# Optimization experiments

Hardware: AMD Instinct MI355X
Metric: run time of the kernel (lower is better)

Reference implementation:

```python
import jax, jax.numpy as jnp
import numpy as np

# Faithful reference for NaiveKmeans._cost / one assignment step of forward:
# squared Euclidean distances (torch.cdist(x, centers)**2) followed by a
# row-wise min (costs) and argmin (cluster indices).
# Note: the original module's host-side while-loop re-seeds centers as
# x[indices] (shape (N,d)), which is a bug that explodes to an NxN cdist;
# the kernel-relevant, well-defined math is this single cdist^2 + min step,
# which we implement here (it is exactly what forward computes before the loop).

def setup_inputs() -> dict:
    key = jax.random.key(0)
    kx, kc = jax.random.split(key)
    x = jax.random.normal(kx, (131072, 128), dtype=jnp.float32)
    centers = jax.random.normal(kc, (1024, 128), dtype=jnp.float32)
    return {"x": x, "centers": centers}


def _sq_cdist(x, c):
    x2 = jnp.sum(x * x, axis=1, keepdims=True)        # [N, 1]
    c2 = jnp.sum(c * c, axis=1)                       # [K]
    d2 = x2 + c2 - 2.0 * (x @ c.T)                    # [N, K]
    return jnp.maximum(d2, 0.0)


def reference(x, centers):
    d2 = _sq_cdist(x, centers)          # [N, K] squared distances
    costs = jnp.min(d2, axis=1)         # [N] per-point cost
    indices = jnp.argmin(d2, axis=1)    # [N] cluster assignment
    return costs, indices
```

## Files before the change

kernel.cpp:

```cpp
#include <hip/hip_runtime.h>


typedef _Float16 f16x8 __attribute__((ext_vector_type(8)));
typedef float    f32x4 __attribute__((ext_vector_type(4)));
typedef unsigned short u16;

constexpr int N = 131072, D = 128, K = 1024;
constexpr int MT = 128;

union H2U { _Float16 h; unsigned short u; };

__device__ inline void gl_lds16(const void* g, void* l) {
  __builtin_amdgcn_global_load_lds(
      (const __attribute__((address_space(1))) unsigned int*)g,
      (__attribute__((address_space(3))) unsigned int*)l, 16, 0, 0);
}

__global__ void prep_centers(const float* __restrict__ centers,
                             u16* __restrict__ Bh, u16* __restrict__ Bl,
                             float* __restrict__ c2) {
  const int wave = threadIdx.x >> 6, lane = threadIdx.x & 63;
  const int c = blockIdx.x * 4 + wave;
  const float2 v = ((const float2*)(centers + (size_t)c * D))[lane];
  float s = v.x * v.x + v.y * v.y;
  #pragma unroll
  for (int off = 32; off; off >>= 1) s += __shfl_xor(s, off, 64);
  if (lane == 0) c2[c] = s;

  H2U h0, h1, l0, l1;
  h0.h = (_Float16)v.x;  l0.h = (_Float16)(v.x - (float)h0.h);
  h1.h = (_Float16)v.y;  l1.h = (_Float16)(v.y - (float)h1.h);
  const int cb = c >> 7, cm = c & 127;
  const int kc = lane >> 4, q = (lane >> 2) & 3, j0 = (lane & 3) * 2;
  const size_t off = (((size_t)(cb * 4 + kc) * 4 + q) * 128 + cm) * 8 + j0;
  *(unsigned*)(Bh + off) = (unsigned)h0.u | ((unsigned)h1.u << 16);
  *(unsigned*)(Bl + off) = (unsigned)l0.u | ((unsigned)l1.u << 16);
}

__global__ __launch_bounds__(256, 2) void kmeans_mfma(
    const float* __restrict__ x,
    const u16* __restrict__ Bh_g, const u16* __restrict__ Bl_g,
    const float* __restrict__ c2g,
    float* __restrict__ out_cost, float* __restrict__ out_idx)
{
  __shared__ __align__(16) u16 smem[40960];
  u16* Ah = smem;
  u16* Al = smem + 16384;

  const int tid = threadIdx.x;
  const int wave = tid >> 6, lane = tid & 63;
  const int wr = wave >> 1, wc = wave & 1;
  const int q = lane >> 4, ln = lane & 15;
  const int m0 = blockIdx.x * MT;

  #pragma unroll
  for (int i = 0; i < 16; ++i) {
    const int flat = i * 256 + tid;
    const int m = flat >> 5, c4 = flat & 31, k0 = c4 * 4;
    const float4 v = *(const float4*)(x + (size_t)(m0 + m) * D + k0);
    const int kc = k0 >> 5, qq = (k0 >> 3) & 3, j0 = k0 & 7;
    const float vv[4] = {v.x, v.y, v.z, v.w};
    H2U h[4], l[4];
    #pragma unroll
    for (int z = 0; z < 4; ++z) {
      h[z].h = (_Float16)vv[z];
      l[z].h = (_Float16)(vv[z] - (float)h[z].h);
    }
    const int off = ((kc * 4 + qq) * 128 + m) * 8 + j0;
    uint2 hp, lp;
    hp.x = h[0].u | ((unsigned)h[1].u << 16); hp.y = h[2].u | ((unsigned)h[3].u << 16);
    lp.x = l[0].u | ((unsigned)l[1].u << 16); lp.y = l[2].u | ((unsigned)l[3].u << 16);
    *(uint2*)(Ah + off) = hp;
    *(uint2*)(Al + off) = lp;
  }
  __syncthreads();

  float x2m = 0.f;
  if (tid < MT) {
    #pragma unroll
    for (int kq = 0; kq < 16; ++kq) {
      const f16x8 hv = *(const f16x8*)(Ah + (kq * 128 + tid) * 8);
      const f16x8 lv = *(const f16x8*)(Al + (kq * 128 + tid) * 8);
      #pragma unroll
      for (int e = 0; e < 8; ++e) {
        const float xv = (float)hv[e] + (float)lv[e];
        x2m += xv * xv;
      }
    }
  }

  auto stageBh = [&](int cc, int p) {
    const size_t gbase = (size_t)cc * 4096;
    u16* buf = smem + 32768 + p * 4096;
    #pragma unroll
    for (int i = 0; i < 2; ++i) {
      const size_t eoff = (size_t)i * 2048 + (size_t)wave * 512;
      gl_lds16(Bh_g + gbase + eoff + (size_t)lane * 8, buf + eoff);
    }
  };
  auto blPtr = [&](int cc, int t) {
    return (const f16x8*)(Bl_g +
        ((size_t)(cc * 4 + q) * 128 + wc * 64 + t * 16 + ln) * 8);
  };

  float bestV[16]; int bestI[16];
  #pragma unroll
  for (int b = 0; b < 16; ++b) { bestV[b] = 3.4e38f; bestI[b] = 0; }

  stageBh(0, 0);
  f16x8 blc[4], bln[4];
  #pragma unroll
  for (int t = 0; t < 4; ++t) blc[t] = *blPtr(0, t);

  for (int ct = 0; ct < 8; ++ct) {
    f32x4 acc[4][4];
    #pragma unroll
    for (int mt = 0; mt < 4; ++mt)
      #pragma unroll
      for (int nt = 0; nt < 4; ++nt)
        acc[mt][nt] = (f32x4){0.f, 0.f, 0.f, 0.f};

    float c2v[4];
    #pragma unroll
    for (int nt = 0; nt < 4; ++nt)
      c2v[nt] = c2g[ct * 128 + wc * 64 + nt * 16 + ln];

    #pragma unroll
    for (int kc = 0; kc < 4; ++kc) {
      const int cc = ct * 4 + kc;
      __syncthreads();
      if (cc < 31) {
        stageBh(cc + 1, (cc + 1) & 1);
        #pragma unroll
        for (int t = 0; t < 4; ++t) bln[t] = *blPtr(cc + 1, t);
      }
      const u16* buf = smem + 32768 + (cc & 1) * 4096;

      f16x8 ah[4], al[4], bh[4];
      #pragma unroll
      for (int t = 0; t < 4; ++t) {
        const int moff = ((kc * 4 + q) * 128 + wr * 64 + t * 16 + ln) * 8;
        ah[t] = *(const f16x8*)(Ah + moff);
        al[t] = *(const f16x8*)(Al + moff);
        bh[t] = *(const f16x8*)(buf + (q * 128 + wc * 64 + t * 16 + ln) * 8);
      }
      #pragma unroll
      for (int mt = 0; mt < 4; ++mt)
        #pragma unroll
        for (int nt = 0; nt < 4; ++nt)
          acc[mt][nt] = __builtin_amdgcn_mfma_f32_16x16x32_f16(ah[mt], bh[nt], acc[mt][nt], 0, 0, 0);
      #pragma unroll
      for (int mt = 0; mt < 4; ++mt)
        #pragma unroll
        for (int nt = 0; nt < 4; ++nt)
          acc[mt][nt] = __builtin_amdgcn_mfma_f32_16x16x32_f16(al[mt], bh[nt], acc[mt][nt], 0, 0, 0);
      #pragma unroll
      for (int mt = 0; mt < 4; ++mt)
        #pragma unroll
        for (int nt = 0; nt < 4; ++nt)
          acc[mt][nt] = __builtin_amdgcn_mfma_f32_16x16x32_f16(ah[mt], blc[nt], acc[mt][nt], 0, 0, 0);
      #pragma unroll
      for (int t = 0; t < 4; ++t) blc[t] = bln[t];
    }

    #pragma unroll
    for (int nt = 0; nt < 4; ++nt) {
      const int n = ct * 128 + wc * 64 + nt * 16 + ln;
      #pragma unroll
      for (int mt = 0; mt < 4; ++mt)
        #pragma unroll
        for (int r = 0; r < 4; ++r) {
          const float s = __builtin_fmaf(-2.f, acc[mt][nt][r], c2v[nt]);
          const int b = mt * 4 + r;
          if (s < bestV[b]) { bestV[b] = s; bestI[b] = n; }
        }
    }
  }

  #pragma unroll
  for (int b = 0; b < 16; ++b) {
    float v = bestV[b]; int idx = bestI[b];
    #pragma unroll
    for (int off = 1; off < 16; off <<= 1) {
      const float ov = __shfl_xor(v, off, 64);
      const int   oi = __shfl_xor(idx, off, 64);
      if (ov < v || (ov == v && oi < idx)) { v = ov; idx = oi; }
    }
    bestV[b] = v; bestI[b] = idx;
  }

  __syncthreads();
  float* redV = (float*)(smem + 32768);
  int*   redI = (int*)(smem + 33280);
  if (ln == 0) {
    #pragma unroll
    for (int b = 0; b < 16; ++b) {
      const int ml = wr * 64 + (b >> 2) * 16 + q * 4 + (b & 3);
      redV[ml * 2 + wc] = bestV[b];
      redI[ml * 2 + wc] = bestI[b];
    }
  }
  __syncthreads();
  if (tid < MT) {
    float v = redV[tid * 2]; int idx = redI[tid * 2];
    const float v1 = redV[tid * 2 + 1]; const int i1 = redI[tid * 2 + 1];
    if (v1 < v || (v1 == v && i1 < idx)) { v = v1; idx = i1; }
    float cost = x2m + v;
    if (cost < 0.f) cost = 0.f;
    out_cost[m0 + tid] = cost;
    out_idx[m0 + tid]  = (float)idx;
  }
}

extern "C" void kernel_launch(void* const* d_in, const int* in_sizes, int n_in,
                              void* d_out, int out_size, void* d_ws, size_t ws_size,
                              hipStream_t stream) {
  const float* x       = (const float*)d_in[0];
  const float* centers = (const float*)d_in[1];
  u16*   Bh = (u16*)d_ws;
  u16*   Bl = Bh + (size_t)K * D;
  float* c2 = (float*)(Bl + (size_t)K * D);
  float* out_cost = (float*)d_out;
  float* out_idx  = out_cost + N;

  prep_centers<<<K / 4, 256, 0, stream>>>(centers, Bh, Bl, c2);
  kmeans_mfma<<<N / MT, 256, 0, stream>>>(x, Bh, Bl, c2, out_cost, out_idx);
}
```

Baseline: 179.4 us.

## Software-pipeline MFMA groups with register double-buffered B and A fragment reads

```diff
diff --git a/kernel.cpp b/kernel.cpp
--- a/kernel.cpp
+++ b/kernel.cpp
@@ -98,84 +98,115 @@
       gl_lds16(Bh_g + gbase + eoff + (size_t)lane * 8, buf + eoff);
     }
   };
-  auto blPtr = [&](int cc, int t) {
-    return (const f16x8*)(Bl_g +
-        ((size_t)(cc * 4 + q) * 128 + wc * 64 + t * 16 + ln) * 8);
-  };
 
   float bestV[16]; int bestI[16];
   #pragma unroll
   for (int b = 0; b < 16; ++b) { bestV[b] = 3.4e38f; bestI[b] = 0; }
 
+  f32x4 acc[4][4];
+  #pragma unroll
+  for (int mt = 0; mt < 4; ++mt)
+    #pragma unroll
+    for (int nt = 0; nt < 4; ++nt)
+      acc[mt][nt] = (f32x4){0.f, 0.f, 0.f, 0.f};
+
+  f16x8 ah[4], al[4];
+  f16x8 bhS[2][4], blS[2][4];
+
+#define READ_B(J, CC)  do {                                                    \
+    const u16* buf_ = smem + 32768 + ((J) & 1) * 4096;                         \
+    _Pragma("unroll")                                                          \
+    for (int t = 0; t < 4; ++t) {                                              \
+      bhS[(J) & 1][t] =                                                        \
+          *(const f16x8*)(buf_ + (q * 128 + wc * 64 + t * 16 + ln) * 8);       \
+      blS[(J) & 1][t] = *(const f16x8*)(Bl_g +                                 \
+          ((size_t)((CC) * 4 + q) * 128 + wc * 64 + t * 16 + ln) * 8);         \
+    }                                                                          \
+  } while (0)
+
+#define READ_A(KC)  do {                                                       \
+    _Pragma("unroll")                                                          \
+    for (int t = 0; t < 4; ++t) {                                              \
+      const int aoff_ = (((KC) * 4 + q) * 128 + wr * 64 + t * 16 + ln) * 8;    \
+      ah[t] = *(const f16x8*)(Ah + aoff_);                                     \
+      al[t] = *(const f16x8*)(Al + aoff_);                                     \
+    }                                                                          \
+  } while (0)
+
+#define MFMA_GROUP(MS)  do {                                                   \
+    _Pragma("unroll")                                                          \
+    for (int mt = 0; mt < 4; ++mt)                                             \
+      _Pragma("unroll")                                                        \
+      for (int nt = 0; nt < 4; ++nt)                                           \
+        acc[mt][nt] = __builtin_amdgcn_mfma_f32_16x16x32_f16(                  \
+            ah[mt], bhS[MS][nt], acc[mt][nt], 0, 0, 0);                        \
+    _Pragma("unroll")                                                          \
+    for (int mt = 0; mt < 4; ++mt)                                             \
+      _Pragma("unroll")                                                        \
+      for (int nt = 0; nt < 4; ++nt)                                           \
+        acc[mt][nt] = __builtin_amdgcn_mfma_f32_16x16x32_f16(                  \
+            al[mt], bhS[MS][nt], acc[mt][nt], 0, 0, 0);                        \
+    _Pragma("unroll")                                                          \
+    for (int mt = 0; mt < 4; ++mt)                                             \
+      _Pragma("unroll")                                                        \
+      for (int nt = 0; nt < 4; ++nt)                                           \
+        acc[mt][nt] = __builtin_amdgcn_mfma_f32_16x16x32_f16(                  \
+            ah[mt], blS[MS][nt], acc[mt][nt], 0, 0, 0);                        \
+  } while (0)
+
+#define EPILOGUE(G)  do {                                                      \
+    _Pragma("unroll")                                                          \
+    for (int nt = 0; nt < 4; ++nt) {                                           \
+      const int n_ = (G) * 128 + wc * 64 + nt * 16 + ln;                       \
+      const float c2v_ = c2g[n_];                                              \
+      _Pragma("unroll")                                                        \
+      for (int mt = 0; mt < 4; ++mt)                                           \
+        _Pragma("unroll")                                                      \
+        for (int r = 0; r < 4; ++r) {                                          \
+          const float s_ = __builtin_fmaf(-2.f, acc[mt][nt][r], c2v_);         \
+          const int b_ = mt * 4 + r;                                           \
+          if (s_ < bestV[b_]) { bestV[b_] = s_; bestI[b_] = n_; }              \
+        }                                                                      \
+    }                                                                          \
+    _Pragma("unroll")                                                          \
+    for (int mt = 0; mt < 4; ++mt)                                             \
+      _Pragma("unroll")                                                        \
+      for (int nt = 0; nt < 4; ++nt)                                           \
+        acc[mt][nt] = (f32x4){0.f, 0.f, 0.f, 0.f};                             \
+  } while (0)
+
   stageBh(0, 0);
-  f16x8 blc[4], bln[4];
-  #pragma unroll
-  for (int t = 0; t < 4; ++t) blc[t] = *blPtr(0, t);
-
-  for (int ct = 0; ct < 8; ++ct) {
-    f32x4 acc[4][4];
-    #pragma unroll
-    for (int mt = 0; mt < 4; ++mt)
-      #pragma unroll
-      for (int nt = 0; nt < 4; ++nt)
-        acc[mt][nt] = (f32x4){0.f, 0.f, 0.f, 0.f};
-
-    float c2v[4];
-    #pragma unroll
-    for (int nt = 0; nt < 4; ++nt)
-      c2v[nt] = c2g[ct * 128 + wc * 64 + nt * 16 + ln];
-
-    #pragma unroll
-    for (int kc = 0; kc < 4; ++kc) {
-      const int cc = ct * 4 + kc;
-      __syncthreads();
-      if (cc < 31) {
-        stageBh(cc + 1, (cc + 1) & 1);
-        #pragma unroll
-        for (int t = 0; t < 4; ++t) bln[t] = *blPtr(cc + 1, t);
-      }
-      const u16* buf = smem + 32768 + (cc & 1) * 4096;
-
-      f16x8 ah[4], al[4], bh[4];
-      #pragma unroll
-      for (int t = 0; t < 4; ++t) {
-        const int moff = ((kc * 4 + q) * 128 + wr * 64 + t * 16 + ln) * 8;
-        ah[t] = *(const f16x8*)(Ah + moff);
-        al[t] = *(const f16x8*)(Al + moff);
-        bh[t] = *(const f16x8*)(buf + (q * 128 + wc * 64 + t * 16 + ln) * 8);
-      }
-      #pragma unroll
-      for (int mt = 0; mt < 4; ++mt)
-        #pragma unroll
-        for (int nt = 0; nt < 4; ++nt)
-          acc[mt][nt] = __builtin_amdgcn_mfma_f32_16x16x32_f16(ah[mt], bh[nt], acc[mt][nt], 0, 0, 0);
-      #pragma unroll
-      for (int mt = 0; mt < 4; ++mt)
-        #pragma unroll
-        for (int nt = 0; nt < 4; ++nt)
-          acc[mt][nt] = __builtin_amdgcn_mfma_f32_16x16x32_f16(al[mt], bh[nt], acc[mt][nt], 0, 0, 0);
-      #pragma unroll
-      for (int mt = 0; mt < 4; ++mt)
-        #pragma unroll
-        for (int nt = 0; nt < 4; ++nt)
-          acc[mt][nt] = __builtin_amdgcn_mfma_f32_16x16x32_f16(ah[mt], blc[nt], acc[mt][nt], 0, 0, 0);
-      #pragma unroll
-      for (int t = 0; t < 4; ++t) blc[t] = bln[t];
-    }
-
-    #pragma unroll
-    for (int nt = 0; nt < 4; ++nt) {
-      const int n = ct * 128 + wc * 64 + nt * 16 + ln;
-      #pragma unroll
-      for (int mt = 0; mt < 4; ++mt)
-        #pragma unroll
-        for (int r = 0; r < 4; ++r) {
-          const float s = __builtin_fmaf(-2.f, acc[mt][nt][r], c2v[nt]);
-          const int b = mt * 4 + r;
-          if (s < bestV[b]) { bestV[b] = s; bestI[b] = n; }
-        }
-    }
-  }
+
+  for (int it = 0; it < 8; ++it) {
+    const int c0 = it * 4;
+    __syncthreads();
+    stageBh(c0 + 1, 1);
+    READ_B(0, c0);
+    if (it > 0) { MFMA_GROUP(1); EPILOGUE(it - 1); }
+    READ_A(0);
+    __syncthreads();
+    stageBh(c0 + 2, 0);
+    READ_B(1, c0 + 1);
+    MFMA_GROUP(0);
+    READ_A(1);
+    __syncthreads();
+    stageBh(c0 + 3, 1);
+    READ_B(0, c0 + 2);
+    MFMA_GROUP(1);
+    READ_A(2);
+    __syncthreads();
+    if (it < 7) stageBh(c0 + 4, 0);
+    READ_B(1, c0 + 3);
+    MFMA_GROUP(0);
+    READ_A(3);
+  }
+  MFMA_GROUP(1);
+  EPILOGUE(7);
+
+#undef READ_B
+#undef READ_A
+#undef MFMA_GROUP
+#undef EPILOGUE
 
   #pragma unroll
   for (int b = 0; b < 16; ++b) {
```

Measured after the change: 180.2 us. Within noise of the previous version (+0.5%).

## Use single-pass fp16 GEMM with error-bound filter and exact rescan of ambiguous rows

Applied to the files above, without the earlier changes.

```diff
diff --git a/kernel.cpp b/kernel.cpp
--- a/kernel.cpp
+++ b/kernel.cpp
@@ -4,6 +4,7 @@
 typedef _Float16 f16x8 __attribute__((ext_vector_type(8)));
 typedef float    f32x4 __attribute__((ext_vector_type(4)));
 typedef unsigned short u16;
+typedef unsigned int   u32;
 
 constexpr int N = 131072, D = 128, K = 1024;
 constexpr int MT = 128;
@@ -18,18 +19,28 @@
 
 __global__ void prep_centers(const float* __restrict__ centers,
                              u16* __restrict__ Bh, u16* __restrict__ Bl,
-                             float* __restrict__ c2) {
+                             float* __restrict__ c2, u32* __restrict__ scal) {
   const int wave = threadIdx.x >> 6, lane = threadIdx.x & 63;
   const int c = blockIdx.x * 4 + wave;
   const float2 v = ((const float2*)(centers + (size_t)c * D))[lane];
-  float s = v.x * v.x + v.y * v.y;
+
+  H2U h0, h1, l0, l1;
+  h0.h = (_Float16)v.x;  float r0 = v.x - (float)h0.h;  l0.h = (_Float16)r0;
+  h1.h = (_Float16)v.y;  float r1 = v.y - (float)h1.h;  l1.h = (_Float16)r1;
+
+  float s  = v.x * v.x + v.y * v.y;
+  float sl = r0 * r0 + r1 * r1;
   #pragma unroll
-  for (int off = 32; off; off >>= 1) s += __shfl_xor(s, off, 64);
-  if (lane == 0) c2[c] = s;
-
-  H2U h0, h1, l0, l1;
-  h0.h = (_Float16)v.x;  l0.h = (_Float16)(v.x - (float)h0.h);
-  h1.h = (_Float16)v.y;  l1.h = (_Float16)(v.y - (float)h1.h);
+  for (int off = 32; off; off >>= 1) {
+    s  += __shfl_xor(s, off, 64);
+    sl += __shfl_xor(sl, off, 64);
+  }
+  if (lane == 0) {
+    c2[c] = s;
+    atomicMax(&scal[0], __float_as_uint(s));
+    atomicMax(&scal[1], __float_as_uint(sl));
+  }
+
   const int cb = c >> 7, cm = c & 127;
   const int kc = lane >> 4, q = (lane >> 2) & 3, j0 = (lane & 3) * 2;
   const size_t off = (((size_t)(cb * 4 + kc) * 4 + q) * 128 + cm) * 8 + j0;
@@ -37,15 +48,15 @@
   *(unsigned*)(Bl + off) = (unsigned)l0.u | ((unsigned)l1.u << 16);
 }
 
-__global__ __launch_bounds__(256, 2) void kmeans_mfma(
-    const float* __restrict__ x,
-    const u16* __restrict__ Bh_g, const u16* __restrict__ Bl_g,
-    const float* __restrict__ c2g,
+__global__ void __launch_bounds__(256, 3) kmeans_p1(
+    const float* __restrict__ x, const u16* __restrict__ Bh_g,
+    const float* __restrict__ c2g, const u32* __restrict__ scal,
+    u32* __restrict__ cnt, u32* __restrict__ worklist,
     float* __restrict__ out_cost, float* __restrict__ out_idx)
 {
-  __shared__ __align__(16) u16 smem[40960];
-  u16* Ah = smem;
-  u16* Al = smem + 16384;
+  __shared__ __align__(16) u16 Ah[16384];
+  __shared__ float x2l[128], Ml[128];
+  __shared__ float redA[256]; __shared__ int redB[256]; __shared__ float redC[256];
 
   const int tid = threadIdx.x;
   const int wave = tid >> 6, lane = tid & 63;
@@ -53,64 +64,53 @@
   const int q = lane >> 4, ln = lane & 15;
   const int m0 = blockIdx.x * MT;
 
+  const float cmax  = sqrtf(__uint_as_float(scal[0]));
+  const float clmax = sqrtf(__uint_as_float(scal[1]));
+
+  {
+    const int m = tid >> 1, half = (tid & 1) * 64;
+    const float* xrow = x + (size_t)(m0 + m) * D + half;
+    float x2p = 0.f, xl2p = 0.f;
+    #pragma unroll
+    for (int i = 0; i < 16; ++i) {
+      const float4 v = *(const float4*)(xrow + i * 4);
+      const int k0 = half + i * 4;
+      const int kq = k0 >> 5, qq = (k0 >> 3) & 3, j0 = k0 & 7;
+      const float vv[4] = {v.x, v.y, v.z, v.w};
+      H2U h[4];
+      #pragma unroll
+      for (int z = 0; z < 4; ++z) {
+        h[z].h = (_Float16)vv[z];
+        const float l = vv[z] - (float)h[z].h;
+        x2p  += vv[z] * vv[z];
+        xl2p += l * l;
+      }
+      uint2 hp;
+      hp.x = h[0].u | ((unsigned)h[1].u << 16);
+      hp.y = h[2].u | ((unsigned)h[3].u << 16);
+      *(uint2*)(Ah + ((kq * 4 + qq) * 128 + m) * 8 + j0) = hp;
+    }
+    const float ox2 = __shfl_xor(x2p, 1, 64);
+    const float oxl = __shfl_xor(xl2p, 1, 64);
+    if ((tid & 1) == 0) {
+      const float X2 = x2p + ox2, XL2 = xl2p + oxl;
+      x2l[m] = X2;
+      const float xn = sqrtf(X2), xln = sqrtf(XL2);
+      Ml[m] = 4.f * (xln * cmax + xn * clmax + xln * clmax) + 0.05f;
+    }
+  }
+  __syncthreads();
+
+  const size_t laneB = ((size_t)q * 128 + wc * 64 + ln) * 8;
+  const u16* bhP = Bh_g + laneB;
+
+  float v1[16], v2[16]; int i1[16];
   #pragma unroll
-  for (int i = 0; i < 16; ++i) {
-    const int flat = i * 256 + tid;
-    const int m = flat >> 5, c4 = flat & 31, k0 = c4 * 4;
-    const float4 v = *(const float4*)(x + (size_t)(m0 + m) * D + k0);
-    const int kc = k0 >> 5, qq = (k0 >> 3) & 3, j0 = k0 & 7;
-    const float vv[4] = {v.x, v.y, v.z, v.w};
-    H2U h[4], l[4];
-    #pragma unroll
-    for (int z = 0; z < 4; ++z) {
-      h[z].h = (_Float16)vv[z];
-      l[z].h = (_Float16)(vv[z] - (float)h[z].h);
-    }
-    const int off = ((kc * 4 + qq) * 128 + m) * 8 + j0;
-    uint2 hp, lp;
-    hp.x = h[0].u | ((unsigned)h[1].u << 16); hp.y = h[2].u | ((unsigned)h[3].u << 16);
-    lp.x = l[0].u | ((unsigned)l[1].u << 16); lp.y = l[2].u | ((unsigned)l[3].u << 16);
-    *(uint2*)(Ah + off) = hp;
-    *(uint2*)(Al + off) = lp;
-  }
-  __syncthreads();
-
-  float x2m = 0.f;
-  if (tid < MT) {
-    #pragma unroll
-    for (int kq = 0; kq < 16; ++kq) {
-      const f16x8 hv = *(const f16x8*)(Ah + (kq * 128 + tid) * 8);
-      const f16x8 lv = *(const f16x8*)(Al + (kq * 128 + tid) * 8);
-      #pragma unroll
-      for (int e = 0; e < 8; ++e) {
-        const float xv = (float)hv[e] + (float)lv[e];
-        x2m += xv * xv;
-      }
-    }
-  }
-
-  auto stageBh = [&](int cc, int p) {
-    const size_t gbase = (size_t)cc * 4096;
-    u16* buf = smem + 32768 + p * 4096;
-    #pragma unroll
-    for (int i = 0; i < 2; ++i) {
-      const size_t eoff = (size_t)i * 2048 + (size_t)wave * 512;
-      gl_lds16(Bh_g + gbase + eoff + (size_t)lane * 8, buf + eoff);
-    }
-  };
-  auto blPtr = [&](int cc, int t) {
-    return (const f16x8*)(Bl_g +
-        ((size_t)(cc * 4 + q) * 128 + wc * 64 + t * 16 + ln) * 8);
-  };
-
-  float bestV[16]; int bestI[16];
+  for (int b = 0; b < 16; ++b) { v1[b] = 3.4e38f; v2[b] = 3.4e38f; i1[b] = 0; }
+
+  f16x8 bhS[2][4];
   #pragma unroll
-  for (int b = 0; b < 16; ++b) { bestV[b] = 3.4e38f; bestI[b] = 0; }
-
-  stageBh(0, 0);
-  f16x8 blc[4], bln[4];
-  #pragma unroll
-  for (int t = 0; t < 4; ++t) blc[t] = *blPtr(0, t);
+  for (int t = 0; t < 4; ++t) bhS[0][t] = *(const f16x8*)(bhP + t * 128);
 
   for (int ct = 0; ct < 8; ++ct) {
     f32x4 acc[4][4];
@@ -128,39 +128,22 @@
     #pragma unroll
     for (int kc = 0; kc < 4; ++kc) {
       const int cc = ct * 4 + kc;
-      __syncthreads();
-      if (cc < 31) {
-        stageBh(cc + 1, (cc + 1) & 1);
-        #pragma unroll
-        for (int t = 0; t < 4; ++t) bln[t] = *blPtr(cc + 1, t);
-      }
-      const u16* buf = smem + 32768 + (cc & 1) * 4096;
-
-      f16x8 ah[4], al[4], bh[4];
-      #pragma unroll
-      for (int t = 0; t < 4; ++t) {
-        const int moff = ((kc * 4 + q) * 128 + wr * 64 + t * 16 + ln) * 8;
-        ah[t] = *(const f16x8*)(Ah + moff);
-        al[t] = *(const f16x8*)(Al + moff);
-        bh[t] = *(const f16x8*)(buf + (q * 128 + wc * 64 + t * 16 + ln) * 8);
-      }
+      const int cur = kc & 1, nxt = cur ^ 1;
+      if (kc < 3 || ct < 7) {
+        const size_t goff = (size_t)(cc + 1) * 4096;
+        #pragma unroll
+        for (int t = 0; t < 4; ++t)
+          bhS[nxt][t] = *(const f16x8*)(bhP + goff + t * 128);
+      }
+      f16x8 ah[4];
+      #pragma unroll
+      for (int t = 0; t < 4; ++t)
+        ah[t] = *(const f16x8*)(Ah + ((kc * 4 + q) * 128 + wr * 64 + t * 16 + ln) * 8);
       #pragma unroll
       for (int mt = 0; mt < 4; ++mt)
         #pragma unroll
         for (int nt = 0; nt < 4; ++nt)
-          acc[mt][nt] = __builtin_amdgcn_mfma_f32_16x16x32_f16(ah[mt], bh[nt], acc[mt][nt], 0, 0, 0);
-      #pragma unroll
-      for (int mt = 0; mt < 4; ++mt)
-        #pragma unroll
-        for (int nt = 0; nt < 4; ++nt)
-          acc[mt][nt] = __builtin_amdgcn_mfma_f32_16x16x32_f16(al[mt], bh[nt], acc[mt][nt], 0, 0, 0);
-      #pragma unroll
-      for (int mt = 0; mt < 4; ++mt)
-        #pragma unroll
-        for (int nt = 0; nt < 4; ++nt)
-          acc[mt][nt] = __builtin_amdgcn_mfma_f32_16x16x32_f16(ah[mt], blc[nt], acc[mt][nt], 0, 0, 0);
-      #pragma unroll
-      for (int t = 0; t < 4; ++t) blc[t] = bln[t];
+          acc[mt][nt] = __builtin_amdgcn_mfma_f32_16x16x32_f16(ah[mt], bhS[cur][nt], acc[mt][nt], 0, 0, 0);
     }
 
     #pragma unroll
@@ -172,43 +155,245 @@
         for (int r = 0; r < 4; ++r) {
           const float s = __builtin_fmaf(-2.f, acc[mt][nt][r], c2v[nt]);
           const int b = mt * 4 + r;
-          if (s < bestV[b]) { bestV[b] = s; bestI[b] = n; }
+          if (s < v1[b]) { v2[b] = v1[b]; v1[b] = s; i1[b] = n; }
+          else if (s < v2[b]) v2[b] = s;
         }
     }
   }
 
   #pragma unroll
   for (int b = 0; b < 16; ++b) {
-    float v = bestV[b]; int idx = bestI[b];
+    float a1 = v1[b], a2 = v2[b]; int ai = i1[b];
     #pragma unroll
     for (int off = 1; off < 16; off <<= 1) {
-      const float ov = __shfl_xor(v, off, 64);
-      const int   oi = __shfl_xor(idx, off, 64);
-      if (ov < v || (ov == v && oi < idx)) { v = ov; idx = oi; }
-    }
-    bestV[b] = v; bestI[b] = idx;
-  }
-
-  __syncthreads();
-  float* redV = (float*)(smem + 32768);
-  int*   redI = (int*)(smem + 33280);
+      const float o1 = __shfl_xor(a1, off, 64);
+      const float o2 = __shfl_xor(a2, off, 64);
+      const int   oi = __shfl_xor(ai, off, 64);
+      float n2;
+      if (o1 < a1 || (o1 == a1 && oi < ai)) { n2 = fminf(a1, o2); a1 = o1; ai = oi; }
+      else                                   { n2 = fminf(o1, a2); }
+      a2 = n2;
+    }
+    v1[b] = a1; v2[b] = a2; i1[b] = ai;
+  }
   if (ln == 0) {
     #pragma unroll
     for (int b = 0; b < 16; ++b) {
       const int ml = wr * 64 + (b >> 2) * 16 + q * 4 + (b & 3);
-      redV[ml * 2 + wc] = bestV[b];
-      redI[ml * 2 + wc] = bestI[b];
+      redA[ml * 2 + wc] = v1[b];
+      redB[ml * 2 + wc] = i1[b];
+      redC[ml * 2 + wc] = v2[b];
     }
   }
   __syncthreads();
   if (tid < MT) {
-    float v = redV[tid * 2]; int idx = redI[tid * 2];
-    const float v1 = redV[tid * 2 + 1]; const int i1 = redI[tid * 2 + 1];
-    if (v1 < v || (v1 == v && i1 < idx)) { v = v1; idx = i1; }
-    float cost = x2m + v;
+    float a1 = redA[tid * 2], a2 = redC[tid * 2]; int ai = redB[tid * 2];
+    const float o1 = redA[tid * 2 + 1], o2 = redC[tid * 2 + 1];
+    const int   oi = redB[tid * 2 + 1];
+    float n2;
+    if (o1 < a1 || (o1 == a1 && oi < ai)) { n2 = fminf(a1, o2); a1 = o1; ai = oi; }
+    else                                   { n2 = fminf(o1, a2); }
+    a2 = n2;
+
+    float cost = x2l[tid] + a1;
     if (cost < 0.f) cost = 0.f;
     out_cost[m0 + tid] = cost;
-    out_idx[m0 + tid]  = (float)idx;
+    out_idx[m0 + tid]  = (float)ai;
+    if (a2 <= a1 + Ml[tid]) {
+      const u32 slot = atomicAdd(cnt, 1u);
+      worklist[slot] = (u32)(m0 + tid);
+    }
+  }
+}
+
+__global__ void __launch_bounds__(256, 2) kmeans_rescan(
+    const float* __restrict__ x,
+    const u16* __restrict__ Bh_g, const u16* __restrict__ Bl_g,
+    const float* __restrict__ c2g, const u32* __restrict__ cnt,
+    const u32* __restrict__ worklist,
+    float* __restrict__ out_cost, float* __restrict__ out_idx)
+{
+  __shared__ __align__(16) u16 smem[40960];
+  __shared__ int pidl[128];
+  u16* Ah = smem;
+  u16* Al = smem + 16384;
+
+  const int tid = threadIdx.x;
+  const int wave = tid >> 6, lane = tid & 63;
+  const int wr = wave >> 1, wc = wave & 1;
+  const int q = lane >> 4, ln = lane & 15;
+  const int count = (int)cnt[0];
+
+  for (int g = blockIdx.x; ; g += 128) {
+    const int base = g * MT;
+    if (base >= count) break;
+    __syncthreads();
+    if (tid < 128) {
+      int wi = base + tid; if (wi >= count) wi = count - 1;
+      pidl[tid] = (int)worklist[wi];
+    }
+    __syncthreads();
+
+    #pragma unroll
+    for (int i = 0; i < 16; ++i) {
+      const int flat = i * 256 + tid;
+      const int m = flat >> 5, c4 = flat & 31, k0 = c4 * 4;
+      const float4 v = *(const float4*)(x + (size_t)pidl[m] * D + k0);
+      const int kc = k0 >> 5, qq = (k0 >> 3) & 3, j0 = k0 & 7;
+      const float vv[4] = {v.x, v.y, v.z, v.w};
+      H2U h[4], l[4];
+      #pragma unroll
+      for (int z = 0; z < 4; ++z) {
+        h[z].h = (_Float16)vv[z];
+        l[z].h = (_Float16)(vv[z] - (float)h[z].h);
+      }
+      const int off = ((kc * 4 + qq) * 128 + m) * 8 + j0;
+      uint2 hp, lp;
+      hp.x = h[0].u | ((unsigned)h[1].u << 16); hp.y = h[2].u | ((unsigned)h[3].u << 16);
+      lp.x = l[0].u | ((unsigned)l[1].u << 16); lp.y = l[2].u | ((unsigned)l[3].u << 16);
+      *(uint2*)(Ah + off) = hp;
+      *(uint2*)(Al + off) = lp;
+    }
+    __syncthreads();
+
+    float x2m = 0.f;
+    if (tid < 128) {
+      #pragma unroll
+      for (int kq = 0; kq < 16; ++kq) {
+        const f16x8 hv = *(const f16x8*)(Ah + (kq * 128 + tid) * 8);
+        const f16x8 lv = *(const f16x8*)(Al + (kq * 128 + tid) * 8);
+        #pragma unroll
+        for (int e = 0; e < 8; ++e) {
+          const float xv = (float)hv[e] + (float)lv[e];
+          x2m += xv * xv;
+        }
+      }
+    }
+
+    const size_t laneB = ((size_t)q * 128 + wc * 64 + ln) * 8;
+    const u16* blP = Bl_g + laneB;
+
+    float bestV[16]; int bestI[16];
+    #pragma unroll
+    for (int b = 0; b < 16; ++b) { bestV[b] = 3.4e38f; bestI[b] = 0; }
+
+    {
+      const size_t eoffb = (size_t)wave * 512;
+      #pragma unroll
+      for (int i = 0; i < 2; ++i)
+        gl_lds16(Bh_g + (size_t)i * 2048 + eoffb + (size_t)lane * 8,
+                 smem + 32768 + i * 2048 + eoffb);
+    }
+    f16x8 blc[4], bln[4];
+    #pragma unroll
+    for (int t = 0; t < 4; ++t) blc[t] = *(const f16x8*)(blP + t * 128);
+
+    for (int ct = 0; ct < 8; ++ct) {
+      f32x4 acc[4][4];
+      #pragma unroll
+      for (int mt = 0; mt < 4; ++mt)
+        #pragma unroll
+        for (int nt = 0; nt < 4; ++nt)
+          acc[mt][nt] = (f32x4){0.f, 0.f, 0.f, 0.f};
+
+      float c2v[4];
+      #pragma unroll
+      for (int nt = 0; nt < 4; ++nt)
+        c2v[nt] = c2g[ct * 128 + wc * 64 + nt * 16 + ln];
+
+      #pragma unroll
+      for (int kc = 0; kc < 4; ++kc) {
+        const int cc = ct * 4 + kc;
+        __syncthreads();
+        if (cc < 31) {
+          const size_t gbase = (size_t)(cc + 1) * 4096;
+          u16* buf = smem + 32768 + ((cc + 1) & 1) * 4096;
+          const size_t eoffb = (size_t)wave * 512;
+          #pragma unroll
+          for (int i = 0; i < 2; ++i)
+            gl_lds16(Bh_g + gbase + (size_t)i * 2048 + eoffb + (size_t)lane * 8,
+                     buf + i * 2048 + eoffb);
+          #pragma unroll
+          for (int t = 0; t < 4; ++t)
+            bln[t] = *(const f16x8*)(blP + gbase + t * 128);
+        }
+        const u16* buf = smem + 32768 + (cc & 1) * 4096;
+
+        f16x8 ah[4], al[4], bh[4];
+        #pragma unroll
+        for (int t = 0; t < 4; ++t) {
+          const int moff = ((kc * 4 + q) * 128 + wr * 64 + t * 16 + ln) * 8;
+          ah[t] = *(const f16x8*)(Ah + moff);
+          al[t] = *(const f16x8*)(Al + moff);
+          bh[t] = *(const f16x8*)(buf + (q * 128 + wc * 64 + t * 16 + ln) * 8);
+        }
+        #pragma unroll
+        for (int mt = 0; mt < 4; ++mt)
+          #pragma unroll
+          for (int nt = 0; nt < 4; ++nt)
+            acc[mt][nt] = __builtin_amdgcn_mfma_f32_16x16x32_f16(ah[mt], bh[nt], acc[mt][nt], 0, 0, 0);
+        #pragma unroll
+        for (int mt = 0; mt < 4; ++mt)
+          #pragma unroll
+          for (int nt = 0; nt < 4; ++nt)
+            acc[mt][nt] = __builtin_amdgcn_mfma_f32_16x16x32_f16(al[mt], bh[nt], acc[mt][nt], 0, 0, 0);
+        #pragma unroll
+        for (int mt = 0; mt < 4; ++mt)
+          #pragma unroll
+          for (int nt = 0; nt < 4; ++nt)
+            acc[mt][nt] = __builtin_amdgcn_mfma_f32_16x16x32_f16(ah[mt], blc[nt], acc[mt][nt], 0, 0, 0);
+        #pragma unroll
+        for (int t = 0; t < 4; ++t) blc[t] = bln[t];
+      }
+
+      #pragma unroll
+      for (int nt = 0; nt < 4; ++nt) {
+        const int n = ct * 128 + wc * 64 + nt * 16 + ln;
+        #pragma unroll
+        for (int mt = 0; mt < 4; ++mt)
+          #pragma unroll
+          for (int r = 0; r < 4; ++r) {
+            const float s = __builtin_fmaf(-2.f, acc[mt][nt][r], c2v[nt]);
+            const int b = mt * 4 + r;
+            if (s < bestV[b]) { bestV[b] = s; bestI[b] = n; }
+          }
+      }
+    }
+
+    #pragma unroll
+    for (int b = 0; b < 16; ++b) {
+      float v = bestV[b]; int idx = bestI[b];
+      #pragma unroll
+      for (int off = 1; off < 16; off <<= 1) {
+        const float ov = __shfl_xor(v, off, 64);
+        const int   oi = __shfl_xor(idx, off, 64);
+        if (ov < v || (ov == v && oi < idx)) { v = ov; idx = oi; }
+      }
+      bestV[b] = v; bestI[b] = idx;
+    }
+
+    __syncthreads();
+    float* redV = (float*)(smem + 32768);
+    int*   redI = (int*)(smem + 33280);
+    if (ln == 0) {
+      #pragma unroll
+      for (int b = 0; b < 16; ++b) {
+        const int ml = wr * 64 + (b >> 2) * 16 + q * 4 + (b & 3);
+        redV[ml * 2 + wc] = bestV[b];
+        redI[ml * 2 + wc] = bestI[b];
+      }
+    }
+    __syncthreads();
+    if (tid < 128 && base + tid < count) {
+      float v = redV[tid * 2]; int idx = redI[tid * 2];
+      const float v1 = redV[tid * 2 + 1]; const int i1 = redI[tid * 2 + 1];
+      if (v1 < v || (v1 == v && i1 < idx)) { v = v1; idx = i1; }
+      float cost = x2m + v;
+      if (cost < 0.f) cost = 0.f;
+      const int p = pidl[tid];
+      out_cost[p] = cost;
+      out_idx[p]  = (float)idx;
+    }
   }
 }
 
@@ -220,9 +405,15 @@
   u16*   Bh = (u16*)d_ws;
   u16*   Bl = Bh + (size_t)K * D;
   float* c2 = (float*)(Bl + (size_t)K * D);
+  u32*   scal = (u32*)(c2 + K);
+  u32*   worklist = scal + 64;
   float* out_cost = (float*)d_out;
   float* out_idx  = out_cost + N;
 
-  prep_centers<<<K / 4, 256, 0, stream>>>(centers, Bh, Bl, c2);
-  kmeans_mfma<<<N / MT, 256, 0, stream>>>(x, Bh, Bl, c2, out_cost, out_idx);
+  hipMemsetAsync(scal, 0, 256, stream);
+  prep_centers<<<K / 4, 256, 0, stream>>>(centers, Bh, Bl, c2, scal);
+  kmeans_p1<<<N / MT, 256, 0, stream>>>(x, Bh, c2, scal, &scal[2], worklist,
+                                        out_cost, out_idx);
+  kmeans_rescan<<<128, 256, 0, stream>>>(x, Bh, Bl, c2, &scal[2], worklist,
+                                         out_cost, out_idx);
 }
```

Measured after the change: 307.2 us. 71.2% more time.
